# Optimization experiments

Hardware: AMD Instinct MI355X
Metric: run time of the kernel (lower is better)

The kernel has to match this reference:

```python
import jax, jax.numpy as jnp
import numpy as np

H = 16  # number of heads (from init_kwargs)
LN_EPS = 1e-5  # torch nn.LayerNorm default


def layer_norm(x, g, b, eps=LN_EPS):
    mu = jnp.mean(x, axis=-1, keepdims=True)
    var = jnp.var(x, axis=-1, keepdims=True)
    return (x - mu) * jax.lax.rsqrt(var + eps) * g + b


def setup_inputs() -> dict:
    key = jax.random.key(0)
    ks = jax.random.split(key, 8)
    B, S, d = 2, 2048, 1024
    s = 0.02  # small init scale keeps softmax logits in a sane range
    return {
        "embed": jax.random.normal(ks[0], (B, S, d), jnp.float32),
        "Wk": jax.random.normal(ks[1], (d, d), jnp.float32) * s,
        "Wq": jax.random.normal(ks[2], (d, d), jnp.float32) * s,
        "Wv": jax.random.normal(ks[3], (d, d), jnp.float32) * s,
        "w1_w": jax.random.normal(ks[4], (4 * d, d), jnp.float32) * s,
        "w1_b": jnp.zeros((4 * d,), jnp.float32),
        "w2_w": jax.random.normal(ks[5], (d, 4 * d), jnp.float32) * s,
        "w2_b": jnp.zeros((d,), jnp.float32),
        "ln_g": jnp.ones((d,), jnp.float32),
        "ln_b": jnp.zeros((d,), jnp.float32),
        "ln2_g": jnp.ones((d,), jnp.float32),
        "ln2_b": jnp.zeros((d,), jnp.float32),
    }


def reference(embed, Wk, Wq, Wv, w1_w, w1_b, w2_w, w2_b, ln_g, ln_b, ln2_g, ln2_b):
    B, S, d = embed.shape
    dh = d // H
    # nn.Linear(d, d, bias=False): y = x @ W.T
    K = embed @ Wk.T
    Q = embed @ Wq.T
    V = embed @ Wv.T
    Qh = Q.reshape(B, S, H, dh)
    Kh = K.reshape(B, S, H, dh)
    Vh = V.reshape(B, S, H, dh)
    # per-head attention, all heads batched: [B, H, S, S]
    scores = jnp.einsum('bshd,bthd->bhst', Qh, Kh) / jnp.sqrt(jnp.float32(dh))
    attn = jax.nn.softmax(scores, axis=-1)
    out = jnp.einsum('bhst,bthd->bshd', attn, Vh).reshape(B, S, d)
    out = layer_norm(out + embed, ln_g, ln_b)          # residual + ln
    hidden = jax.nn.silu(out @ w1_w.T + w1_b)          # FFN with silu gate
    out2 = hidden @ w2_w.T + w2_b
    return layer_norm(out2 + out, ln2_g, ln2_b)        # residual + ln2
```

## Files before the change

kernel.cpp:

```cpp
#include <hip/hip_runtime.h>
#include <hip/hip_bf16.h>
#include <stdint.h>

typedef __attribute__((ext_vector_type(8))) __bf16 bf16x8;
typedef __attribute__((ext_vector_type(4))) float f32x4;
typedef __attribute__((ext_vector_type(16))) float f32x16;
typedef __attribute__((ext_vector_type(8))) uint16_t u16x8;

__device__ inline uint16_t f2bf(float x) {
  union { float f; uint32_t u; } v; v.f = x;
  uint32_t r = v.u + 0x7fffu + ((v.u >> 16) & 1u);
  return (uint16_t)(r >> 16);
}
__device__ inline float bf2f(uint16_t x) {
  union { uint32_t u; float f; } v; v.u = (uint32_t)x << 16;
  return v.f;
}

#define MFMA16(a, b, c) __builtin_amdgcn_mfma_f32_16x16x32_bf16(a, b, c, 0, 0, 0)
#define MFMA32(a, b, c) __builtin_amdgcn_mfma_f32_32x32x16_bf16(a, b, c, 0, 0, 0)
#define GLOAD16(g, l) __builtin_amdgcn_global_load_lds((const __attribute__((address_space(1))) void*)(g), (__attribute__((address_space(3))) void*)(l), 16, 0, 0)

#if __has_builtin(__builtin_amdgcn_exp2f)
#define EXP2(x) __builtin_amdgcn_exp2f(x)
#else
#define EXP2(x) exp2f(x)
#endif

__device__ inline uint32_t cvtpk_bf16(float lo, float hi) {
  uint32_t r;
  asm("v_cvt_pk_bf16_f32 %0, %1, %2" : "=v"(r) : "v"(lo), "v"(hi));
  return r;
}
__device__ inline void perm32swap(uint32_t& a, uint32_t& b) {
  asm volatile("v_permlane32_swap_b32 %0, %1" : "+v"(a), "+v"(b));
}

__global__ void cast_all(const float* __restrict__ embed, const float* __restrict__ Wq,
                         const float* __restrict__ Wk, const float* __restrict__ Wv,
                         const float* __restrict__ w1w, const float* __restrict__ w2w,
                         uint16_t* __restrict__ xbf, uint16_t* __restrict__ wqkv,
                         uint16_t* __restrict__ w1b, uint16_t* __restrict__ w2b) {
  const int i = (blockIdx.x * 256 + threadIdx.x) * 4;
  const float* src; uint16_t* dst; float sc = 1.f; int off;
  if (i < 4194304)       { src = embed; dst = xbf;            off = i; }
  else if (i < 5242880)  { src = Wq;  dst = wqkv;             off = i - 4194304; sc = 0.125f * 1.44269504f; }
  else if (i < 6291456)  { src = Wk;  dst = wqkv + 1048576;   off = i - 5242880; }
  else if (i < 7340032)  { src = Wv;  dst = wqkv + 2097152;   off = i - 6291456; }
  else if (i < 11534336) { src = w1w; dst = w1b;              off = i - 7340032; }
  else                   { src = w2w; dst = w2b;              off = i - 11534336; }
  float4 v = *(const float4*)(src + off);
  ushort4 o;
  o.x = f2bf(v.x * sc); o.y = f2bf(v.y * sc);
  o.z = f2bf(v.z * sc); o.w = f2bf(v.w * sc);
  *(ushort4*)(dst + off) = o;
}

template <int EPI>
__global__ void gemm_bt(const uint16_t* __restrict__ A, const uint16_t* __restrict__ Bm,
                        void* __restrict__ C0, void* __restrict__ C1,
                        void* __restrict__ C2, void* __restrict__ C3,
                        const float* __restrict__ bias, int N, int K, int ldk) {
  __shared__ uint16_t Albs[128 * 64];
  __shared__ uint16_t Blbs[128 * 64];
  const int tid = threadIdx.x;
  const int l = tid & 63, w = tid >> 6;
  const int wr = w >> 1, wc = w & 1;

  const int gx = gridDim.x;
  const int nwg = gx * gridDim.y;
  const int orig = blockIdx.y * gx + blockIdx.x;
  const int wg = (orig & 7) * (nwg >> 3) + (orig >> 3);
  const int row0 = (wg % gx) * 128;
  const int col0 = (wg / gx) * 128;

  const int kz = blockIdx.z;
  const uint16_t* Ap = A + (size_t)kz * K;
  const uint16_t* Bp = Bm + (size_t)kz * K;
  void* Co = kz == 0 ? C0 : (kz == 1 ? C1 : (kz == 2 ? C2 : C3));

  const int srow8 = l >> 3;
  const int sgcol = ((l & 7) ^ srow8) * 8;
  const int lr = l & 15, l4 = l >> 4;

  f32x4 acc[4][4] = {};

  const int nk = K >> 6;
  for (int kt = 0; kt < nk; ++kt) {
    __syncthreads();
    const int k0 = kt * 64 + sgcol;
#pragma unroll
    for (int i = 0; i < 4; ++i) {
      GLOAD16(Ap + (size_t)(row0 + i * 32 + w * 8 + srow8) * ldk + k0,
              Albs + (i * 32 + w * 8) * 64);
      GLOAD16(Bp + (size_t)(col0 + i * 32 + w * 8 + srow8) * ldk + k0,
              Blbs + (i * 32 + w * 8) * 64);
    }
    __syncthreads();
#pragma unroll
    for (int kk = 0; kk < 2; ++kk) {
      bf16x8 af[4], bfr[4];
#pragma unroll
      for (int m = 0; m < 4; ++m) {
        const int r = wr * 64 + m * 16 + lr;
        af[m] = *(const bf16x8*)((const char*)Albs + r * 128 + (((kk * 4 + l4) ^ (r & 7)) << 4));
      }
#pragma unroll
      for (int n = 0; n < 4; ++n) {
        const int r = wc * 64 + n * 16 + lr;
        bfr[n] = *(const bf16x8*)((const char*)Blbs + r * 128 + (((kk * 4 + l4) ^ (r & 7)) << 4));
      }
#pragma unroll
      for (int m = 0; m < 4; ++m)
#pragma unroll
        for (int n = 0; n < 4; ++n)
          acc[m][n] = MFMA16(af[m], bfr[n], acc[m][n]);
    }
  }

  float bias_r[4];
  if (EPI == 1 || (EPI == 2 && kz == 0)) {
#pragma unroll
    for (int n = 0; n < 4; ++n) bias_r[n] = bias[col0 + wc * 64 + n * 16 + lr];
  }
#pragma unroll
  for (int m = 0; m < 4; ++m)
#pragma unroll
    for (int n = 0; n < 4; ++n) {
      const int rbase = row0 + wr * 64 + m * 16 + (l4 << 2);
      const int c = col0 + wc * 64 + n * 16 + lr;
      if (EPI == 1) {
#pragma unroll
        for (int v = 0; v < 4; ++v) {
          float x = acc[m][n][v] + bias_r[n];
          float s = x / (1.f + __expf(-x));
          ((uint16_t*)Co)[(size_t)(rbase + v) * N + c] = f2bf(s);
        }
      } else if (EPI == 2) {
#pragma unroll
        for (int v = 0; v < 4; ++v) {
          float x = acc[m][n][v];
          if (kz == 0) x += bias_r[n];
          ((float*)Co)[(size_t)(rbase + v) * N + c] = x;
        }
      } else {
        if (c < 2048) {
#pragma unroll
          for (int v = 0; v < 4; ++v)
            ((uint16_t*)C0)[(size_t)(rbase + v) * 2048 + c] = f2bf(acc[m][n][v]);
        } else {
          const int d = c - 2048;
          union { uint16_t u[4]; uint64_t q; } pk;
#pragma unroll
          for (int v = 0; v < 4; ++v) pk.u[v] = f2bf(acc[m][n][v]);
          const int bb = rbase >> 11, srow = rbase & 2047;
          uint16_t* vt = (uint16_t*)C1;
          *(uint64_t*)(vt + ((size_t)((bb << 4) + (d >> 6)) * 64 + (d & 63)) * 2048 + srow) = pk.q;
        }
      }
    }
}

__global__ __launch_bounds__(256, 2) void attn_kernel(const uint16_t* __restrict__ qk,
                                                      const uint16_t* __restrict__ Vt,
                                                      uint16_t* __restrict__ out) {
  __shared__ uint16_t Klds[2][4096];
  __shared__ uint16_t Vlds[2][4096];
  const int tid = threadIdx.x;
  const int l = tid & 63, w = tid >> 6;
  const int lq = l & 31, hi = l >> 5;
  const int qt = blockIdx.x, bh = blockIdx.y;
  const size_t rowbase = (size_t)(bh >> 4) * 2048;
  const int h = bh & 15;
  const int hq = h * 64, hk = 1024 + h * 64;

  const int qrow = qt * 128 + w * 32 + lq;
  bf16x8 qf[4];
  {
    const uint16_t* qp = qk + (rowbase + qrow) * 2048 + hq + hi * 8;
#pragma unroll
    for (int c = 0; c < 4; ++c) qf[c] = *(const bf16x8*)(qp + c * 16);
  }

  const int srow = w * 8 + (l >> 3);
  const int gcol = 8 * ((l & 7) ^ (l >> 3));

  f32x16 ot[2];
#pragma unroll
  for (int r = 0; r < 16; ++r) { ot[0][r] = 0.f; ot[1][r] = 0.f; }
  float m_run = -1e30f, l_run = 0.f;

  auto STAGE = [&](int buf, int kv0) {
#pragma unroll
    for (int p = 0; p < 2; ++p) {
      const uint16_t* srcK = qk + (rowbase + kv0 + p * 32 + srow) * 2048 + hk + gcol;
      GLOAD16(srcK, (char*)&Klds[buf][0] + p * 4096 + w * 1024);
      const uint16_t* srcV = Vt + ((size_t)bh * 64 + p * 32 + srow) * 2048 + kv0 + gcol;
      GLOAD16(srcV, (char*)&Vlds[buf][0] + p * 4096 + w * 1024);
    }
  };

  STAGE(0, 0);
  int cur = 0;
  const int swz = (lq & 7) << 4;

  for (int t = 0; t < 32; ++t) {
    asm volatile("s_waitcnt vmcnt(0)" ::: "memory");
    __builtin_amdgcn_s_barrier();
    if (t < 31) STAGE(cur ^ 1, (t + 1) * 64);

    f32x16 st[2];
#pragma unroll
    for (int b = 0; b < 2; ++b) {
      f32x16 acm;
#pragma unroll
      for (int r = 0; r < 16; ++r) acm[r] = 0.f;
      __builtin_amdgcn_s_setprio(1);
#pragma unroll
      for (int c = 0; c < 4; ++c) {
        const int cbk = (c * 32 + hi * 16) ^ swz;
        bf16x8 kf = *(const bf16x8*)((const char*)&Klds[cur][0] + (b * 32 + lq) * 128 + cbk);
        acm = MFMA32(kf, qf[c], acm);
      }
      __builtin_amdgcn_s_setprio(0);
      st[b] = acm;
    }

    float mloc = st[0][0];
#pragma unroll
    for (int r = 1; r < 16; ++r) mloc = fmaxf(mloc, st[0][r]);
#pragma unroll
    for (int r = 0; r < 16; ++r) mloc = fmaxf(mloc, st[1][r]);
    const float mtile = fmaxf(mloc, __shfl_xor(mloc, 32, 64));
    if (!__all(mtile <= m_run + 8.f)) {
      const float mnew = fmaxf(m_run, mtile);
      const float sc = EXP2(m_run - mnew);
      m_run = mnew;
      l_run *= sc;
#pragma unroll
      for (int r = 0; r < 16; ++r) { ot[0][r] *= sc; ot[1][r] *= sc; }
    }
    float p0[16], p1[16];
    float rsum = 0.f;
#pragma unroll
    for (int r = 0; r < 16; ++r) { p0[r] = EXP2(st[0][r] - m_run); rsum += p0[r]; }
#pragma unroll
    for (int r = 0; r < 16; ++r) { p1[r] = EXP2(st[1][r] - m_run); rsum += p1[r]; }
    l_run += rsum + __shfl_xor(rsum, 32, 64);

    uint32_t pa[4][4];
#pragma unroll
    for (int b = 0; b < 2; ++b) {
      const float* pp = b ? p1 : p0;
#pragma unroll
      for (int c = 0; c < 2; ++c) {
        uint32_t a0 = cvtpk_bf16(pp[8 * c + 0], pp[8 * c + 1]);
        uint32_t a1 = cvtpk_bf16(pp[8 * c + 2], pp[8 * c + 3]);
        uint32_t b0 = cvtpk_bf16(pp[8 * c + 4], pp[8 * c + 5]);
        uint32_t b1 = cvtpk_bf16(pp[8 * c + 6], pp[8 * c + 7]);
        perm32swap(a0, b0);
        perm32swap(a1, b1);
        pa[b * 2 + c][0] = a0; pa[b * 2 + c][1] = a1;
        pa[b * 2 + c][2] = b0; pa[b * 2 + c][3] = b1;
      }
    }

    __builtin_amdgcn_s_setprio(1);
#pragma unroll
    for (int ks = 0; ks < 4; ++ks) {
      bf16x8 pf = *(bf16x8*)&pa[ks][0];
#pragma unroll
      for (int db = 0; db < 2; ++db) {
        const int cbk = (ks * 32 + hi * 16) ^ swz;
        bf16x8 vf = *(const bf16x8*)((const char*)&Vlds[cur][0] + (db * 32 + lq) * 128 + cbk);
        ot[db] = MFMA32(vf, pf, ot[db]);
      }
    }
    __builtin_amdgcn_s_setprio(0);
    cur ^= 1;
  }

  const float linv = 1.f / l_run;
  uint16_t* orow = out + (rowbase + qrow) * 1024 + h * 64;
#pragma unroll
  for (int db = 0; db < 2; ++db)
#pragma unroll
    for (int m = 0; m < 4; ++m) {
      union { uint16_t u[4]; uint64_t q; } pk;
#pragma unroll
      for (int v = 0; v < 4; ++v) pk.u[v] = f2bf(ot[db][4 * m + v] * linv);
      *(uint64_t*)(orow + db * 32 + 8 * m + 4 * hi) = pk.q;
    }
}

__global__ __launch_bounds__(256) void ln_kernel(const float* __restrict__ x0p,
                                                 const uint16_t* __restrict__ x0b,
                                                 const float* __restrict__ x1p,
                                                 const float* __restrict__ x2p,
                                                 const float* __restrict__ x3p,
                                                 const float* __restrict__ x4p,
                                                 const float* __restrict__ g,
                                                 const float* __restrict__ b,
                                                 float* __restrict__ y32,
                                                 uint16_t* __restrict__ y16) {
  const int row = blockIdx.x;
  const int t = threadIdx.x;
  const int l = t & 63, w = t >> 6;
  float x0, x1, x2, x3;
  if (x0b) {
    ushort4 vb4 = *((const ushort4*)(x0b + (size_t)row * 1024) + t);
    x0 = bf2f(vb4.x); x1 = bf2f(vb4.y); x2 = bf2f(vb4.z); x3 = bf2f(vb4.w);
  } else {
    float4 va = *((const float4*)(x0p + (size_t)row * 1024) + t);
    x0 = va.x; x1 = va.y; x2 = va.z; x3 = va.w;
  }
  {
    float4 vb = *((const float4*)(x1p + (size_t)row * 1024) + t);
    x0 += vb.x; x1 += vb.y; x2 += vb.z; x3 += vb.w;
  }
  if (x2p) {
    float4 vc = *((const float4*)(x2p + (size_t)row * 1024) + t);
    x0 += vc.x; x1 += vc.y; x2 += vc.z; x3 += vc.w;
  }
  if (x3p) {
    float4 vc = *((const float4*)(x3p + (size_t)row * 1024) + t);
    x0 += vc.x; x1 += vc.y; x2 += vc.z; x3 += vc.w;
  }
  if (x4p) {
    float4 vc = *((const float4*)(x4p + (size_t)row * 1024) + t);
    x0 += vc.x; x1 += vc.y; x2 += vc.z; x3 += vc.w;
  }
  float s = x0 + x1 + x2 + x3;
  float q = x0 * x0 + x1 * x1 + x2 * x2 + x3 * x3;
#pragma unroll
  for (int off = 1; off < 64; off <<= 1) {
    s += __shfl_xor(s, off, 64);
    q += __shfl_xor(q, off, 64);
  }
  __shared__ float red[8];
  if (l == 0) { red[w] = s; red[w + 4] = q; }
  __syncthreads();
  s = red[0] + red[1] + red[2] + red[3];
  q = red[4] + red[5] + red[6] + red[7];
  const float mu = s * (1.f / 1024.f);
  const float var = q * (1.f / 1024.f) - mu * mu;
  const float rstd = rsqrtf(var + 1e-5f);
  float4 vg = *((const float4*)g + t);
  float4 vbb = *((const float4*)b + t);
  float y0 = (x0 - mu) * rstd * vg.x + vbb.x;
  float y1 = (x1 - mu) * rstd * vg.y + vbb.y;
  float y2 = (x2 - mu) * rstd * vg.z + vbb.z;
  float y3 = (x3 - mu) * rstd * vg.w + vbb.w;
  *((float4*)(y32 + (size_t)row * 1024) + t) = make_float4(y0, y1, y2, y3);
  if (y16) {
    union { uint16_t u[4]; uint64_t v; } o;
    o.u[0] = f2bf(y0); o.u[1] = f2bf(y1); o.u[2] = f2bf(y2); o.u[3] = f2bf(y3);
    *((uint64_t*)(y16 + (size_t)row * 1024) + t) = o.v;
  }
}

extern "C" void kernel_launch(void* const* d_in, const int* in_sizes, int n_in,
                              void* d_out, int out_size, void* d_ws, size_t ws_size,
                              hipStream_t stream) {
  const float* embed = (const float*)d_in[0];
  const float* Wk = (const float*)d_in[1];
  const float* Wq = (const float*)d_in[2];
  const float* Wv = (const float*)d_in[3];
  const float* w1w = (const float*)d_in[4];
  const float* w1bias = (const float*)d_in[5];
  const float* w2w = (const float*)d_in[6];
  const float* w2bias = (const float*)d_in[7];
  const float* lng = (const float*)d_in[8];
  const float* lnb = (const float*)d_in[9];
  const float* ln2g = (const float*)d_in[10];
  const float* ln2b = (const float*)d_in[11];

  char* ws = (char*)d_ws;
  uint16_t* qk   = (uint16_t*)(ws);
  uint16_t* abf  = (uint16_t*)(ws + 16777216);
  uint16_t* xbf  = (uint16_t*)(ws + 25165824);
  uint16_t* wqkv = (uint16_t*)(ws + 33554432);
  uint16_t* w1b  = (uint16_t*)(ws + 39845888);
  uint16_t* w2b  = (uint16_t*)(ws + 48234496);
  float*    attf = (float*)(ws + 56623104);
  float*    yf   = (float*)(ws + 73400320);
  uint16_t* hid  = (uint16_t*)(ws + 90177536);
  uint16_t* Vt   = (uint16_t*)(ws + 90177536);
  float*    part1 = (float*)qk;
  float*    part2 = (float*)(ws + 25165824);
  float*    part3 = (float*)d_out;

  cast_all<<<dim3(15360), dim3(256), 0, stream>>>(embed, Wq, Wk, Wv, w1w, w2w,
                                                  xbf, wqkv, w1b, w2b);

  gemm_bt<3><<<dim3(32, 24), dim3(256), 0, stream>>>(xbf, wqkv, qk, Vt, nullptr, nullptr,
                                                     nullptr, 3072, 1024, 1024);
  attn_kernel<<<dim3(16, 32), dim3(256), 0, stream>>>(qk, Vt, abf);
  ln_kernel<<<dim3(4096), dim3(256), 0, stream>>>(nullptr, abf, embed, nullptr, nullptr, nullptr,
                                                  lng, lnb, yf, xbf);
  gemm_bt<1><<<dim3(32, 32), dim3(256), 0, stream>>>(xbf, w1b, hid, nullptr, nullptr, nullptr,
                                                     w1bias, 4096, 1024, 1024);
  gemm_bt<2><<<dim3(32, 8, 4), dim3(256), 0, stream>>>(hid, w2b, attf, part1, part2, part3,
                                                       w2bias, 1024, 1024, 4096);
  ln_kernel<<<dim3(4096), dim3(256), 0, stream>>>(attf, nullptr, part1, part2, part3, yf,
                                                  ln2g, ln2b, (float*)d_out, nullptr);
}
```

Before: 219.9 us.

## Process two query blocks per attention wave and store split-K partials as bf16

The attention kernel now gives each wave 64 query rows (two 32-row blocks) that share every K/V LDS fragment. This halves the grid and the K/V staging traffic per query, at the cost of more registers and lower occupancy (launch bounds drop to one block). The split-K FFN2 GEMM now writes its non-first partial sums as bf16 instead of fp32, and the final layernorm reads them as bf16. That cuts partial-sum write and read bandwidth but lowers the precision of the summed output.

```diff
diff --git a/kernel.cpp b/kernel.cpp
--- a/kernel.cpp
+++ b/kernel.cpp
@@ -137,11 +137,14 @@
           ((uint16_t*)Co)[(size_t)(rbase + v) * N + c] = f2bf(s);
         }
       } else if (EPI == 2) {
-#pragma unroll
-        for (int v = 0; v < 4; ++v) {
-          float x = acc[m][n][v];
-          if (kz == 0) x += bias_r[n];
-          ((float*)Co)[(size_t)(rbase + v) * N + c] = x;
+        if (kz == 0) {
+#pragma unroll
+          for (int v = 0; v < 4; ++v)
+            ((float*)Co)[(size_t)(rbase + v) * N + c] = acc[m][n][v] + bias_r[n];
+        } else {
+#pragma unroll
+          for (int v = 0; v < 4; ++v)
+            ((uint16_t*)Co)[(size_t)(rbase + v) * N + c] = f2bf(acc[m][n][v]);
         }
       } else {
         if (c < 2048) {
@@ -161,7 +164,7 @@
     }
 }
 
-__global__ __launch_bounds__(256, 2) void attn_kernel(const uint16_t* __restrict__ qk,
+__global__ __launch_bounds__(256, 1) void attn_kernel(const uint16_t* __restrict__ qk,
                                                       const uint16_t* __restrict__ Vt,
                                                       uint16_t* __restrict__ out) {
   __shared__ uint16_t Klds[2][4096];
@@ -174,21 +177,24 @@
   const int h = bh & 15;
   const int hq = h * 64, hk = 1024 + h * 64;
 
-  const int qrow = qt * 128 + w * 32 + lq;
-  bf16x8 qf[4];
-  {
+  bf16x8 qf[2][4];
+#pragma unroll
+  for (int qb = 0; qb < 2; ++qb) {
+    const int qrow = qt * 256 + w * 64 + qb * 32 + lq;
     const uint16_t* qp = qk + (rowbase + qrow) * 2048 + hq + hi * 8;
 #pragma unroll
-    for (int c = 0; c < 4; ++c) qf[c] = *(const bf16x8*)(qp + c * 16);
+    for (int c = 0; c < 4; ++c) qf[qb][c] = *(const bf16x8*)(qp + c * 16);
   }
 
   const int srow = w * 8 + (l >> 3);
   const int gcol = 8 * ((l & 7) ^ (l >> 3));
 
-  f32x16 ot[2];
-#pragma unroll
-  for (int r = 0; r < 16; ++r) { ot[0][r] = 0.f; ot[1][r] = 0.f; }
-  float m_run = -1e30f, l_run = 0.f;
+  f32x16 ot[2][2];
+#pragma unroll
+  for (int qb = 0; qb < 2; ++qb)
+#pragma unroll
+    for (int r = 0; r < 16; ++r) { ot[qb][0][r] = 0.f; ot[qb][1][r] = 0.f; }
+  float m_run[2] = {-1e30f, -1e30f}, l_run[2] = {0.f, 0.f};
 
   auto STAGE = [&](int buf, int kv0) {
 #pragma unroll
@@ -209,96 +215,105 @@
     __builtin_amdgcn_s_barrier();
     if (t < 31) STAGE(cur ^ 1, (t + 1) * 64);
 
-    f32x16 st[2];
+    f32x16 st[2][2];
 #pragma unroll
     for (int b = 0; b < 2; ++b) {
-      f32x16 acm;
-#pragma unroll
-      for (int r = 0; r < 16; ++r) acm[r] = 0.f;
+      f32x16 s0, s1;
+#pragma unroll
+      for (int r = 0; r < 16; ++r) { s0[r] = 0.f; s1[r] = 0.f; }
       __builtin_amdgcn_s_setprio(1);
 #pragma unroll
       for (int c = 0; c < 4; ++c) {
         const int cbk = (c * 32 + hi * 16) ^ swz;
         bf16x8 kf = *(const bf16x8*)((const char*)&Klds[cur][0] + (b * 32 + lq) * 128 + cbk);
-        acm = MFMA32(kf, qf[c], acm);
+        s0 = MFMA32(kf, qf[0][c], s0);
+        s1 = MFMA32(kf, qf[1][c], s1);
       }
       __builtin_amdgcn_s_setprio(0);
-      st[b] = acm;
-    }
-
-    float mloc = st[0][0];
-#pragma unroll
-    for (int r = 1; r < 16; ++r) mloc = fmaxf(mloc, st[0][r]);
-#pragma unroll
-    for (int r = 0; r < 16; ++r) mloc = fmaxf(mloc, st[1][r]);
-    const float mtile = fmaxf(mloc, __shfl_xor(mloc, 32, 64));
-    if (!__all(mtile <= m_run + 8.f)) {
-      const float mnew = fmaxf(m_run, mtile);
-      const float sc = EXP2(m_run - mnew);
-      m_run = mnew;
-      l_run *= sc;
-#pragma unroll
-      for (int r = 0; r < 16; ++r) { ot[0][r] *= sc; ot[1][r] *= sc; }
-    }
-    float p0[16], p1[16];
-    float rsum = 0.f;
-#pragma unroll
-    for (int r = 0; r < 16; ++r) { p0[r] = EXP2(st[0][r] - m_run); rsum += p0[r]; }
-#pragma unroll
-    for (int r = 0; r < 16; ++r) { p1[r] = EXP2(st[1][r] - m_run); rsum += p1[r]; }
-    l_run += rsum + __shfl_xor(rsum, 32, 64);
-
-    uint32_t pa[4][4];
-#pragma unroll
-    for (int b = 0; b < 2; ++b) {
-      const float* pp = b ? p1 : p0;
-#pragma unroll
-      for (int c = 0; c < 2; ++c) {
-        uint32_t a0 = cvtpk_bf16(pp[8 * c + 0], pp[8 * c + 1]);
-        uint32_t a1 = cvtpk_bf16(pp[8 * c + 2], pp[8 * c + 3]);
-        uint32_t b0 = cvtpk_bf16(pp[8 * c + 4], pp[8 * c + 5]);
-        uint32_t b1 = cvtpk_bf16(pp[8 * c + 6], pp[8 * c + 7]);
-        perm32swap(a0, b0);
-        perm32swap(a1, b1);
-        pa[b * 2 + c][0] = a0; pa[b * 2 + c][1] = a1;
-        pa[b * 2 + c][2] = b0; pa[b * 2 + c][3] = b1;
-      }
+      st[0][b] = s0; st[1][b] = s1;
+    }
+
+    uint32_t pa[2][4][4];
+#pragma unroll
+    for (int qb = 0; qb < 2; ++qb) {
+      float mloc = st[qb][0][0];
+#pragma unroll
+      for (int r = 1; r < 16; ++r) mloc = fmaxf(mloc, st[qb][0][r]);
+#pragma unroll
+      for (int r = 0; r < 16; ++r) mloc = fmaxf(mloc, st[qb][1][r]);
+      const float mtile = fmaxf(mloc, __shfl_xor(mloc, 32, 64));
+      if (!__all(mtile <= m_run[qb] + 8.f)) {
+        const float mnew = fmaxf(m_run[qb], mtile);
+        const float sc = EXP2(m_run[qb] - mnew);
+        m_run[qb] = mnew;
+        l_run[qb] *= sc;
+#pragma unroll
+        for (int r = 0; r < 16; ++r) { ot[qb][0][r] *= sc; ot[qb][1][r] *= sc; }
+      }
+      float rsum = 0.f;
+#pragma unroll
+      for (int b = 0; b < 2; ++b)
+#pragma unroll
+        for (int r = 0; r < 16; ++r) {
+          float e = EXP2(st[qb][b][r] - m_run[qb]);
+          st[qb][b][r] = e;
+          rsum += e;
+        }
+      l_run[qb] += rsum + __shfl_xor(rsum, 32, 64);
+
+#pragma unroll
+      for (int b = 0; b < 2; ++b)
+#pragma unroll
+        for (int c = 0; c < 2; ++c) {
+          uint32_t a0 = cvtpk_bf16(st[qb][b][8 * c + 0], st[qb][b][8 * c + 1]);
+          uint32_t a1 = cvtpk_bf16(st[qb][b][8 * c + 2], st[qb][b][8 * c + 3]);
+          uint32_t b0 = cvtpk_bf16(st[qb][b][8 * c + 4], st[qb][b][8 * c + 5]);
+          uint32_t b1 = cvtpk_bf16(st[qb][b][8 * c + 6], st[qb][b][8 * c + 7]);
+          perm32swap(a0, b0);
+          perm32swap(a1, b1);
+          pa[qb][b * 2 + c][0] = a0; pa[qb][b * 2 + c][1] = a1;
+          pa[qb][b * 2 + c][2] = b0; pa[qb][b * 2 + c][3] = b1;
+        }
     }
 
     __builtin_amdgcn_s_setprio(1);
 #pragma unroll
     for (int ks = 0; ks < 4; ++ks) {
-      bf16x8 pf = *(bf16x8*)&pa[ks][0];
 #pragma unroll
       for (int db = 0; db < 2; ++db) {
         const int cbk = (ks * 32 + hi * 16) ^ swz;
         bf16x8 vf = *(const bf16x8*)((const char*)&Vlds[cur][0] + (db * 32 + lq) * 128 + cbk);
-        ot[db] = MFMA32(vf, pf, ot[db]);
+        ot[0][db] = MFMA32(vf, *(bf16x8*)&pa[0][ks][0], ot[0][db]);
+        ot[1][db] = MFMA32(vf, *(bf16x8*)&pa[1][ks][0], ot[1][db]);
       }
     }
     __builtin_amdgcn_s_setprio(0);
     cur ^= 1;
   }
 
-  const float linv = 1.f / l_run;
-  uint16_t* orow = out + (rowbase + qrow) * 1024 + h * 64;
-#pragma unroll
-  for (int db = 0; db < 2; ++db)
-#pragma unroll
-    for (int m = 0; m < 4; ++m) {
-      union { uint16_t u[4]; uint64_t q; } pk;
-#pragma unroll
-      for (int v = 0; v < 4; ++v) pk.u[v] = f2bf(ot[db][4 * m + v] * linv);
-      *(uint64_t*)(orow + db * 32 + 8 * m + 4 * hi) = pk.q;
-    }
+#pragma unroll
+  for (int qb = 0; qb < 2; ++qb) {
+    const float linv = 1.f / l_run[qb];
+    const int qrow = qt * 256 + w * 64 + qb * 32 + lq;
+    uint16_t* orow = out + (rowbase + qrow) * 1024 + h * 64;
+#pragma unroll
+    for (int db = 0; db < 2; ++db)
+#pragma unroll
+      for (int m = 0; m < 4; ++m) {
+        union { uint16_t u[4]; uint64_t q; } pk;
+#pragma unroll
+        for (int v = 0; v < 4; ++v) pk.u[v] = f2bf(ot[qb][db][4 * m + v] * linv);
+        *(uint64_t*)(orow + db * 32 + 8 * m + 4 * hi) = pk.q;
+      }
+  }
 }
 
 __global__ __launch_bounds__(256) void ln_kernel(const float* __restrict__ x0p,
                                                  const uint16_t* __restrict__ x0b,
                                                  const float* __restrict__ x1p,
-                                                 const float* __restrict__ x2p,
-                                                 const float* __restrict__ x3p,
-                                                 const float* __restrict__ x4p,
+                                                 const uint16_t* __restrict__ xb1,
+                                                 const uint16_t* __restrict__ xb2,
+                                                 const uint16_t* __restrict__ xb3,
                                                  const float* __restrict__ g,
                                                  const float* __restrict__ b,
                                                  float* __restrict__ y32,
@@ -318,17 +333,17 @@
     float4 vb = *((const float4*)(x1p + (size_t)row * 1024) + t);
     x0 += vb.x; x1 += vb.y; x2 += vb.z; x3 += vb.w;
   }
-  if (x2p) {
-    float4 vc = *((const float4*)(x2p + (size_t)row * 1024) + t);
-    x0 += vc.x; x1 += vc.y; x2 += vc.z; x3 += vc.w;
-  }
-  if (x3p) {
-    float4 vc = *((const float4*)(x3p + (size_t)row * 1024) + t);
-    x0 += vc.x; x1 += vc.y; x2 += vc.z; x3 += vc.w;
-  }
-  if (x4p) {
-    float4 vc = *((const float4*)(x4p + (size_t)row * 1024) + t);
-    x0 += vc.x; x1 += vc.y; x2 += vc.z; x3 += vc.w;
+  if (xb1) {
+    ushort4 vb4 = *((const ushort4*)(xb1 + (size_t)row * 1024) + t);
+    x0 += bf2f(vb4.x); x1 += bf2f(vb4.y); x2 += bf2f(vb4.z); x3 += bf2f(vb4.w);
+  }
+  if (xb2) {
+    ushort4 vb4 = *((const ushort4*)(xb2 + (size_t)row * 1024) + t);
+    x0 += bf2f(vb4.x); x1 += bf2f(vb4.y); x2 += bf2f(vb4.z); x3 += bf2f(vb4.w);
+  }
+  if (xb3) {
+    ushort4 vb4 = *((const ushort4*)(xb3 + (size_t)row * 1024) + t);
+    x0 += bf2f(vb4.x); x1 += bf2f(vb4.y); x2 += bf2f(vb4.z); x3 += bf2f(vb4.w);
   }
   float s = x0 + x1 + x2 + x3;
   float q = x0 * x0 + x1 * x1 + x2 * x2 + x3 * x3;
@@ -386,22 +401,22 @@
   float*    yf   = (float*)(ws + 73400320);
   uint16_t* hid  = (uint16_t*)(ws + 90177536);
   uint16_t* Vt   = (uint16_t*)(ws + 90177536);
-  float*    part1 = (float*)qk;
-  float*    part2 = (float*)(ws + 25165824);
-  float*    part3 = (float*)d_out;
+  uint16_t* part1b = qk;
+  uint16_t* part2b = (uint16_t*)(ws + 25165824);
+  uint16_t* part3b = (uint16_t*)(ws + 33554432);
 
   cast_all<<<dim3(15360), dim3(256), 0, stream>>>(embed, Wq, Wk, Wv, w1w, w2w,
                                                   xbf, wqkv, w1b, w2b);
 
   gemm_bt<3><<<dim3(32, 24), dim3(256), 0, stream>>>(xbf, wqkv, qk, Vt, nullptr, nullptr,
                                                      nullptr, 3072, 1024, 1024);
-  attn_kernel<<<dim3(16, 32), dim3(256), 0, stream>>>(qk, Vt, abf);
+  attn_kernel<<<dim3(8, 32), dim3(256), 0, stream>>>(qk, Vt, abf);
   ln_kernel<<<dim3(4096), dim3(256), 0, stream>>>(nullptr, abf, embed, nullptr, nullptr, nullptr,
                                                   lng, lnb, yf, xbf);
   gemm_bt<1><<<dim3(32, 32), dim3(256), 0, stream>>>(xbf, w1b, hid, nullptr, nullptr, nullptr,
                                                      w1bias, 4096, 1024, 1024);
-  gemm_bt<2><<<dim3(32, 8, 4), dim3(256), 0, stream>>>(hid, w2b, attf, part1, part2, part3,
+  gemm_bt<2><<<dim3(32, 8, 4), dim3(256), 0, stream>>>(hid, w2b, attf, part1b, part2b, part3b,
                                                        w2bias, 1024, 1024, 4096);
-  ln_kernel<<<dim3(4096), dim3(256), 0, stream>>>(attf, nullptr, part1, part2, part3, yf,
+  ln_kernel<<<dim3(4096), dim3(256), 0, stream>>>(attf, nullptr, yf, part1b, part2b, part3b,
                                                   ln2g, ln2b, (float*)d_out, nullptr);
 }
```

After: 231.1 us. +5.1%, slower.

## Split attention KV range across two blocks and store FFN split-K partials in bf16

Applied to the files above, without the earlier changes.

The attention kernel now splits the 2048-key range into two halves along a new grid dimension. Each half writes unnormalized outputs plus its running max and sum, and a new combine kernel merges the halves with rescaled weights. This doubles the attention grid to fill more compute units and shortens each block's serial loop, at the cost of an extra pass over the outputs. Separately, the FFN2 split-K partials are stored as bf16 instead of fp32, and the bias is added in the final layernorm. This halves partial-sum traffic but adds rounding error from storing the unnormalized partial outputs in bf16.

```diff
diff --git a/kernel.cpp b/kernel.cpp
--- a/kernel.cpp
+++ b/kernel.cpp
@@ -119,7 +119,7 @@
   }
 
   float bias_r[4];
-  if (EPI == 1 || (EPI == 2 && kz == 0)) {
+  if (EPI == 1) {
 #pragma unroll
     for (int n = 0; n < 4; ++n) bias_r[n] = bias[col0 + wc * 64 + n * 16 + lr];
   }
@@ -138,11 +138,8 @@
         }
       } else if (EPI == 2) {
 #pragma unroll
-        for (int v = 0; v < 4; ++v) {
-          float x = acc[m][n][v];
-          if (kz == 0) x += bias_r[n];
-          ((float*)Co)[(size_t)(rbase + v) * N + c] = x;
-        }
+        for (int v = 0; v < 4; ++v)
+          ((uint16_t*)Co)[(size_t)(rbase + v) * N + c] = f2bf(acc[m][n][v]);
       } else {
         if (c < 2048) {
 #pragma unroll
@@ -163,16 +160,20 @@
 
 __global__ __launch_bounds__(256, 2) void attn_kernel(const uint16_t* __restrict__ qk,
                                                       const uint16_t* __restrict__ Vt,
-                                                      uint16_t* __restrict__ out) {
+                                                      uint16_t* __restrict__ Op0,
+                                                      uint16_t* __restrict__ Op1,
+                                                      float* __restrict__ ml) {
   __shared__ uint16_t Klds[2][4096];
   __shared__ uint16_t Vlds[2][4096];
   const int tid = threadIdx.x;
   const int l = tid & 63, w = tid >> 6;
   const int lq = l & 31, hi = l >> 5;
-  const int qt = blockIdx.x, bh = blockIdx.y;
+  const int qt = blockIdx.x, bh = blockIdx.y, z = blockIdx.z;
   const size_t rowbase = (size_t)(bh >> 4) * 2048;
   const int h = bh & 15;
   const int hq = h * 64, hk = 1024 + h * 64;
+  const int kvbase = z * 1024;
+  uint16_t* Op = z ? Op1 : Op0;
 
   const int qrow = qt * 128 + w * 32 + lq;
   bf16x8 qf[4];
@@ -200,14 +201,14 @@
     }
   };
 
-  STAGE(0, 0);
+  STAGE(0, kvbase);
   int cur = 0;
   const int swz = (lq & 7) << 4;
 
-  for (int t = 0; t < 32; ++t) {
+  for (int t = 0; t < 16; ++t) {
     asm volatile("s_waitcnt vmcnt(0)" ::: "memory");
     __builtin_amdgcn_s_barrier();
-    if (t < 31) STAGE(cur ^ 1, (t + 1) * 64);
+    if (t < 15) STAGE(cur ^ 1, kvbase + (t + 1) * 64);
 
     f32x16 st[2];
 #pragma unroll
@@ -280,25 +281,54 @@
     cur ^= 1;
   }
 
-  const float linv = 1.f / l_run;
-  uint16_t* orow = out + (rowbase + qrow) * 1024 + h * 64;
+  uint16_t* orow = Op + (rowbase + qrow) * 1024 + h * 64;
 #pragma unroll
   for (int db = 0; db < 2; ++db)
 #pragma unroll
     for (int m = 0; m < 4; ++m) {
       union { uint16_t u[4]; uint64_t q; } pk;
 #pragma unroll
-      for (int v = 0; v < 4; ++v) pk.u[v] = f2bf(ot[db][4 * m + v] * linv);
+      for (int v = 0; v < 4; ++v) pk.u[v] = f2bf(ot[db][4 * m + v]);
       *(uint64_t*)(orow + db * 32 + 8 * m + 4 * hi) = pk.q;
     }
+  if (l < 32) {
+    const size_t mi = ((size_t)(z * 32 + bh) * 2048 + qrow) * 2;
+    *(float2*)(ml + mi) = make_float2(m_run, l_run);
+  }
+}
+
+__global__ __launch_bounds__(256) void attn_combine(const uint16_t* __restrict__ O0,
+                                                    const uint16_t* __restrict__ O1,
+                                                    const float* __restrict__ ml,
+                                                    uint16_t* __restrict__ out) {
+  const int row = blockIdx.x;
+  const int t = threadIdx.x;
+  const int h = t >> 4;
+  const int b = row >> 11, q = row & 2047;
+  const int bh = b * 16 + h;
+  float2 ml0 = *(const float2*)(ml + ((size_t)bh * 2048 + q) * 2);
+  float2 ml1 = *(const float2*)(ml + ((size_t)(32 + bh) * 2048 + q) * 2);
+  const float m = fmaxf(ml0.x, ml1.x);
+  const float w0 = EXP2(ml0.x - m), w1 = EXP2(ml1.x - m);
+  const float linv = 1.f / (ml0.y * w0 + ml1.y * w1);
+  ushort4 a = *((const ushort4*)(O0 + (size_t)row * 1024) + t);
+  ushort4 c = *((const ushort4*)(O1 + (size_t)row * 1024) + t);
+  ushort4 o;
+  o.x = f2bf((bf2f(a.x) * w0 + bf2f(c.x) * w1) * linv);
+  o.y = f2bf((bf2f(a.y) * w0 + bf2f(c.y) * w1) * linv);
+  o.z = f2bf((bf2f(a.z) * w0 + bf2f(c.z) * w1) * linv);
+  o.w = f2bf((bf2f(a.w) * w0 + bf2f(c.w) * w1) * linv);
+  *((ushort4*)(out + (size_t)row * 1024) + t) = o;
 }
 
 __global__ __launch_bounds__(256) void ln_kernel(const float* __restrict__ x0p,
                                                  const uint16_t* __restrict__ x0b,
                                                  const float* __restrict__ x1p,
-                                                 const float* __restrict__ x2p,
-                                                 const float* __restrict__ x3p,
-                                                 const float* __restrict__ x4p,
+                                                 const uint16_t* __restrict__ xb1,
+                                                 const uint16_t* __restrict__ xb2,
+                                                 const uint16_t* __restrict__ xb3,
+                                                 const uint16_t* __restrict__ xb4,
+                                                 const float* __restrict__ abias,
                                                  const float* __restrict__ g,
                                                  const float* __restrict__ b,
                                                  float* __restrict__ y32,
@@ -314,21 +344,29 @@
     float4 va = *((const float4*)(x0p + (size_t)row * 1024) + t);
     x0 = va.x; x1 = va.y; x2 = va.z; x3 = va.w;
   }
-  {
+  if (x1p) {
     float4 vb = *((const float4*)(x1p + (size_t)row * 1024) + t);
     x0 += vb.x; x1 += vb.y; x2 += vb.z; x3 += vb.w;
   }
-  if (x2p) {
-    float4 vc = *((const float4*)(x2p + (size_t)row * 1024) + t);
-    x0 += vc.x; x1 += vc.y; x2 += vc.z; x3 += vc.w;
-  }
-  if (x3p) {
-    float4 vc = *((const float4*)(x3p + (size_t)row * 1024) + t);
-    x0 += vc.x; x1 += vc.y; x2 += vc.z; x3 += vc.w;
-  }
-  if (x4p) {
-    float4 vc = *((const float4*)(x4p + (size_t)row * 1024) + t);
-    x0 += vc.x; x1 += vc.y; x2 += vc.z; x3 += vc.w;
+  if (xb1) {
+    ushort4 vb4 = *((const ushort4*)(xb1 + (size_t)row * 1024) + t);
+    x0 += bf2f(vb4.x); x1 += bf2f(vb4.y); x2 += bf2f(vb4.z); x3 += bf2f(vb4.w);
+  }
+  if (xb2) {
+    ushort4 vb4 = *((const ushort4*)(xb2 + (size_t)row * 1024) + t);
+    x0 += bf2f(vb4.x); x1 += bf2f(vb4.y); x2 += bf2f(vb4.z); x3 += bf2f(vb4.w);
+  }
+  if (xb3) {
+    ushort4 vb4 = *((const ushort4*)(xb3 + (size_t)row * 1024) + t);
+    x0 += bf2f(vb4.x); x1 += bf2f(vb4.y); x2 += bf2f(vb4.z); x3 += bf2f(vb4.w);
+  }
+  if (xb4) {
+    ushort4 vb4 = *((const ushort4*)(xb4 + (size_t)row * 1024) + t);
+    x0 += bf2f(vb4.x); x1 += bf2f(vb4.y); x2 += bf2f(vb4.z); x3 += bf2f(vb4.w);
+  }
+  if (abias) {
+    float4 vb = *((const float4*)abias + t);
+    x0 += vb.x; x1 += vb.y; x2 += vb.z; x3 += vb.w;
   }
   float s = x0 + x1 + x2 + x3;
   float q = x0 * x0 + x1 * x1 + x2 * x2 + x3 * x3;
@@ -382,26 +420,31 @@
   uint16_t* wqkv = (uint16_t*)(ws + 33554432);
   uint16_t* w1b  = (uint16_t*)(ws + 39845888);
   uint16_t* w2b  = (uint16_t*)(ws + 48234496);
-  float*    attf = (float*)(ws + 56623104);
+  uint16_t* Op1  = (uint16_t*)(ws + 56623104);
+  float*    ml   = (float*)(ws + 65011712);
   float*    yf   = (float*)(ws + 73400320);
   uint16_t* hid  = (uint16_t*)(ws + 90177536);
   uint16_t* Vt   = (uint16_t*)(ws + 90177536);
-  float*    part1 = (float*)qk;
-  float*    part2 = (float*)(ws + 25165824);
-  float*    part3 = (float*)d_out;
+  uint16_t* part0b = (uint16_t*)(ws + 56623104);
+  uint16_t* part1b = qk;
+  uint16_t* part2b = (uint16_t*)(ws + 25165824);
+  uint16_t* part3b = (uint16_t*)(ws + 33554432);
 
   cast_all<<<dim3(15360), dim3(256), 0, stream>>>(embed, Wq, Wk, Wv, w1w, w2w,
                                                   xbf, wqkv, w1b, w2b);
 
   gemm_bt<3><<<dim3(32, 24), dim3(256), 0, stream>>>(xbf, wqkv, qk, Vt, nullptr, nullptr,
                                                      nullptr, 3072, 1024, 1024);
-  attn_kernel<<<dim3(16, 32), dim3(256), 0, stream>>>(qk, Vt, abf);
-  ln_kernel<<<dim3(4096), dim3(256), 0, stream>>>(nullptr, abf, embed, nullptr, nullptr, nullptr,
+  attn_kernel<<<dim3(16, 32, 2), dim3(256), 0, stream>>>(qk, Vt, abf, Op1, ml);
+  attn_combine<<<dim3(4096), dim3(256), 0, stream>>>(abf, Op1, ml, abf);
+  ln_kernel<<<dim3(4096), dim3(256), 0, stream>>>(nullptr, abf, embed, nullptr, nullptr,
+                                                  nullptr, nullptr, nullptr,
                                                   lng, lnb, yf, xbf);
   gemm_bt<1><<<dim3(32, 32), dim3(256), 0, stream>>>(xbf, w1b, hid, nullptr, nullptr, nullptr,
                                                      w1bias, 4096, 1024, 1024);
-  gemm_bt<2><<<dim3(32, 8, 4), dim3(256), 0, stream>>>(hid, w2b, attf, part1, part2, part3,
-                                                       w2bias, 1024, 1024, 4096);
-  ln_kernel<<<dim3(4096), dim3(256), 0, stream>>>(attf, nullptr, part1, part2, part3, yf,
+  gemm_bt<2><<<dim3(32, 8, 4), dim3(256), 0, stream>>>(hid, w2b, part0b, part1b, part2b, part3b,
+                                                       nullptr, 1024, 1024, 4096);
+  ln_kernel<<<dim3(4096), dim3(256), 0, stream>>>(yf, nullptr, nullptr, part0b, part1b,
+                                                  part2b, part3b, w2bias,
                                                   ln2g, ln2b, (float*)d_out, nullptr);
 }
```

After: 216.6 us. No clear change (-1.5%).
